# Optimization experiments

Hardware: AMD Instinct MI355X
Metric: run time of the kernel (lower is better)

## Reference

```python
import jax, jax.numpy as jnp
import numpy as np
from functools import partial

TAU = 2.0       # membrane time constant
V_TH = 1.0      # firing threshold
SLOPE = 10.0    # surrogate sigmoid slope (matches rate_encode's 10*)
T = 10          # time_window
H = 12          # num_heads


def lif_step(v, I):
    """One LIF update: leaky integrate, surrogate spike, multiplicative reset."""
    v = v + (I - v) / TAU
    spk = jax.nn.sigmoid(SLOPE * (v - V_TH))
    v = v * (1.0 - spk)
    return spk, v


def setup_inputs() -> dict:
    key = jax.random.key(0)
    ks = jax.random.split(key, 5)
    B, S, E = 8, 1024, 768
    scale = 1.0 / np.sqrt(E)
    x = jax.random.uniform(ks[0], (B, S, E), dtype=jnp.float32)
    Wq = jax.random.normal(ks[1], (E, E), dtype=jnp.float32) * scale
    Wk = jax.random.normal(ks[2], (E, E), dtype=jnp.float32) * scale
    Wv = jax.random.normal(ks[3], (E, E), dtype=jnp.float32) * scale
    Wo = jax.random.normal(ks[4], (E, E), dtype=jnp.float32) * scale
    zb = jnp.zeros((E,), dtype=jnp.float32)
    return {"x": x, "Wq": Wq, "bq": zb, "Wk": Wk, "bk": zb,
            "Wv": Wv, "bv": zb, "Wo": Wo, "bo": zb}


def reference(x, Wq, bq, Wk, bk, Wv, bv, Wo, bo):
    B, S, E = x.shape
    D = E // H
    # rate encoding probability (x assumed in [0,1] range, clipped)
    p = jnp.clip(x, 0.0, 1.0)  # [B,S,E]

    def step(carry, t):
        vq, vk, vv, Qa, Ka, Va = carry
        inp = jax.nn.sigmoid(SLOPE * (p * T - t))  # [B,S,E] spikes at step t
        qs, vq = lif_step(vq, inp @ Wq.T + bq)
        ks, vk = lif_step(vk, inp @ Wk.T + bk)
        vs, vv = lif_step(vv, inp @ Wv.T + bv)
        return (vq, vk, vv, Qa + qs, Ka + ks, Va + vs), None

    z = jnp.zeros((B, S, E), dtype=x.dtype)
    t_idx = jnp.arange(T, dtype=x.dtype)
    (vq, vk, vv, Q, K, V), _ = jax.lax.scan(step, (z, z, z, z, z, z), t_idx)

    # split heads: [B,S,E] -> [B,H,S,D]
    Qh = Q.reshape(B, S, H, D)
    Kh = K.reshape(B, S, H, D)
    Vh = V.reshape(B, S, H, D)
    scores = jnp.einsum('bqhd,bkhd->bhqk', Qh, Kh) / np.sqrt(D)
    attn = jax.nn.softmax(scores, axis=-1)
    out_h = jnp.einsum('bhqk,bkhd->bqhd', attn, Vh)  # [B,S,H,D]
    out = out_h.reshape(B, S, E)
    # output LIF projection with fresh (zero) state
    out_spk, _ = lif_step(jnp.zeros_like(out), out @ Wo.T + bo)
    return out_spk
```

## Files before the change

### kernel.cpp

```cpp
#include <hip/hip_runtime.h>
#include <math.h>

constexpr int B_ = 8, S_ = 1024, E_ = 768, H_ = 12, D_ = 64, T_ = 10;
constexpr int N_ = B_ * S_;
constexpr int NE_ = N_ * E_;
constexpr int WE_ = E_ * E_;

typedef __attribute__((ext_vector_type(8))) short bf16x8;
typedef __attribute__((ext_vector_type(4))) float f32x4;

#define MFMA16(a,b,c) __builtin_amdgcn_mfma_f32_16x16x32_bf16(a,b,c,0,0,0)

__device__ __forceinline__ float sigm(float z){ return 1.f/(1.f+__expf(-z)); }
__device__ __forceinline__ unsigned short f2bf(float f){
    unsigned int u = __float_as_uint(f);
    u += 0x7FFFu + ((u>>16)&1u);
    return (unsigned short)(u>>16);
}
__device__ __forceinline__ float bf2f(unsigned short h){
    return __uint_as_float(((unsigned int)h)<<16);
}
__device__ __forceinline__ void gl16(const void* g, void* l){
    __builtin_amdgcn_global_load_lds((const __attribute__((address_space(1))) unsigned int*)g,
                                     (__attribute__((address_space(3))) unsigned int*)l, 16, 0, 0);
}

__global__ __launch_bounds__(256) void encode_k(const float* __restrict__ x,
                                                unsigned short* __restrict__ enc){
    const int i = blockIdx.x*256 + threadIdx.x;
    const float4 a = ((const float4*)x)[2*i];
    const float4 b = ((const float4*)x)[2*i+1];
    float p[8] = {a.x,a.y,a.z,a.w,b.x,b.y,b.z,b.w};
#pragma unroll
    for (int e=0;e<8;++e) p[e] = 100.f*fminf(fmaxf(p[e],0.f),1.f);
#pragma unroll
    for (int t=0;t<T_;++t){
        unsigned int w[4];
#pragma unroll
        for (int e=0;e<4;++e){
            unsigned short u0 = f2bf(sigm(p[2*e]   - 10.f*(float)t));
            unsigned short u1 = f2bf(sigm(p[2*e+1] - 10.f*(float)t));
            w[e] = (unsigned int)u0 | ((unsigned int)u1<<16);
        }
        ((uint4*)(enc + (long)t*NE_))[i] = make_uint4(w[0],w[1],w[2],w[3]);
    }
}

__global__ __launch_bounds__(256) void wsplit_k(const float* __restrict__ Wq, const float* __restrict__ Wk,
        const float* __restrict__ Wv, const float* __restrict__ Wo,
        unsigned short* __restrict__ whi, unsigned short* __restrict__ wlo){
    int gi = blockIdx.x*256 + threadIdx.x;
    int z = gi / (WE_/8);
    int r = gi % (WE_/8);
    const float* W = z==0?Wq : z==1?Wk : z==2?Wv : Wo;
    const float4 a = ((const float4*)W)[2*r];
    const float4 b = ((const float4*)W)[2*r+1];
    float f[8]={a.x,a.y,a.z,a.w,b.x,b.y,b.z,b.w};
    unsigned int h[4], l[4];
#pragma unroll
    for (int e=0;e<4;++e){
        unsigned short h0=f2bf(f[2*e]),   l0=f2bf(f[2*e]  -bf2f(h0));
        unsigned short h1=f2bf(f[2*e+1]), l1=f2bf(f[2*e+1]-bf2f(h1));
        h[e] = (unsigned)h0 | ((unsigned)h1<<16);
        l[e] = (unsigned)l0 | ((unsigned)l1<<16);
    }
    ((uint4*)(whi + (long)z*WE_))[r] = make_uint4(h[0],h[1],h[2],h[3]);
    ((uint4*)(wlo + (long)z*WE_))[r] = make_uint4(l[0],l[1],l[2],l[3]);
}

__global__ __launch_bounds__(256,2) void qkv_k(const unsigned short* __restrict__ enc,
        const unsigned short* __restrict__ whi,
        const float* __restrict__ bq, const float* __restrict__ bk, const float* __restrict__ bv,
        float* __restrict__ Qf, float* __restrict__ Kf, float* __restrict__ Vf){
    const int z = blockIdx.z;
    const unsigned short* Wh = whi + (long)z*WE_;
    const float* bias = z==0?bq : z==1?bk : bv;
    float* Out = z==0?Qf : z==1?Kf : Vf;
    const int row0 = blockIdx.x*128, col0 = blockIdx.y*64;

    __shared__ unsigned short Ab[128*64];
    __shared__ unsigned short Bh[64*64];

    const int tid = threadIdx.x, lane = tid&63, wid = tid>>6;
    const int l15 = lane&15, l4 = lane>>4, l7 = lane&7;
    const int wr = wid>>1, wc = wid&1;

    int aSrc[4], bSrc[2];
#pragma unroll
    for (int s=0;s<4;++s){
        int idx = (wid + s*4)*64 + lane;
        int row = idx>>3, ch = idx&7;
        aSrc[s] = (row0+row)*E_ + ((ch ^ (row&7))<<3);
    }
#pragma unroll
    for (int s=0;s<2;++s){
        int idx = (wid + s*4)*64 + lane;
        int row = idx>>3, ch = idx&7;
        bSrc[s] = (col0+row)*E_ + ((ch ^ (row&7))<<3);
    }

    const int aBase = (wr*64 + l15)*128;
    const int bBase = (wc*32 + l15)*128;
    const int sw[2] = { ((l4^l7)<<4), ((((4+l4))^l7)<<4) };

    f32x4 acc[4][2];
    float vm[4][2][4] = {};
    float qa[4][2][4] = {};
    float bn[2];
#pragma unroll
    for (int n=0;n<2;++n) bn[n] = bias[col0 + wc*32 + n*16 + l15];
    const f32x4 zero4 = {0.f,0.f,0.f,0.f};

    for (int t=0;t<T_;++t){
        const long tb = (long)t*NE_;
#pragma unroll
        for (int m=0;m<4;++m)
#pragma unroll
            for (int n=0;n<2;++n) acc[m][n] = zero4;
        for (int kt=0;kt<12;++kt){
            const int k0 = kt*64;
            __syncthreads();
#pragma unroll
            for (int s=0;s<4;++s)
                gl16(enc + tb + aSrc[s] + k0, &Ab[(wid+s*4)*512]);
#pragma unroll
            for (int s=0;s<2;++s)
                gl16(Wh + bSrc[s] + k0, &Bh[(wid+s*4)*512]);
            __syncthreads();
#pragma unroll
            for (int kk=0;kk<2;++kk){
                bf16x8 af[4], fbh[2];
#pragma unroll
                for (int m=0;m<4;++m)
                    af[m] = *(const bf16x8*)((const char*)Ab + aBase + m*2048 + sw[kk]);
#pragma unroll
                for (int n=0;n<2;++n)
                    fbh[n] = *(const bf16x8*)((const char*)Bh + bBase + n*2048 + sw[kk]);
#pragma unroll
                for (int m=0;m<4;++m)
#pragma unroll
                    for (int n=0;n<2;++n)
                        acc[m][n] = MFMA16(af[m], fbh[n], acc[m][n]);
            }
        }
#pragma unroll
        for (int m=0;m<4;++m)
#pragma unroll
            for (int n=0;n<2;++n)
#pragma unroll
                for (int j=0;j<4;++j){
                    float I = acc[m][n][j] + bn[n];
                    float v = (vm[m][n][j] + I)*0.5f;
                    float s = sigm(10.f*v - 10.f);
                    vm[m][n][j] = v*(1.f - s);
                    qa[m][n][j] += s;
                }
    }
#pragma unroll
    for (int m=0;m<4;++m)
#pragma unroll
        for (int n=0;n<2;++n)
#pragma unroll
            for (int j=0;j<4;++j){
                int row = row0 + wr*64 + m*16 + l4*4 + j;
                int col = col0 + wc*32 + n*16 + l15;
                Out[(long)row*E_ + col] = qa[m][n][j];
            }
}

__global__ __launch_bounds__(256) void splitqk_k(const float* __restrict__ Qf, const float* __restrict__ Kf,
        unsigned short* __restrict__ Qh, unsigned short* __restrict__ Ql,
        unsigned short* __restrict__ Kh, unsigned short* __restrict__ Kl){
    const long gi = (long)blockIdx.x*256 + threadIdx.x;
    const float* src = blockIdx.y==0 ? Qf : Kf;
    unsigned short* oh = blockIdx.y==0 ? Qh : Kh;
    unsigned short* ol = blockIdx.y==0 ? Ql : Kl;
    const float4 a = ((const float4*)src)[2*gi];
    const float4 b = ((const float4*)src)[2*gi+1];
    float f[8]={a.x,a.y,a.z,a.w,b.x,b.y,b.z,b.w};
    unsigned int hw[4], lw[4];
#pragma unroll
    for (int e=0;e<4;++e){
        unsigned short h0=f2bf(f[2*e]),   l0=f2bf(f[2*e]  -bf2f(h0));
        unsigned short h1=f2bf(f[2*e+1]), l1=f2bf(f[2*e+1]-bf2f(h1));
        hw[e] = (unsigned)h0 | ((unsigned)h1<<16);
        lw[e] = (unsigned)l0 | ((unsigned)l1<<16);
    }
    ((uint4*)oh)[gi] = make_uint4(hw[0],hw[1],hw[2],hw[3]);
    ((uint4*)ol)[gi] = make_uint4(lw[0],lw[1],lw[2],lw[3]);
}

__global__ __launch_bounds__(256) void vtrans_k(const float* __restrict__ Vf,
        unsigned short* __restrict__ Vth, unsigned short* __restrict__ Vtl){
    __shared__ unsigned short lh[64][68], ll[64][68];
    const int tid = threadIdx.x;
    const long base = ((long)blockIdx.z*S_ + blockIdx.x*64)*E_ + blockIdx.y*64;

    {
        const int key = tid>>2, dq = tid&3;
        const float* p = Vf + base + (long)key*E_ + dq*16;
        float4 v0=((const float4*)p)[0], v1=((const float4*)p)[1];
        float4 v2=((const float4*)p)[2], v3=((const float4*)p)[3];
        float f[16]={v0.x,v0.y,v0.z,v0.w,v1.x,v1.y,v1.z,v1.w,
                     v2.x,v2.y,v2.z,v2.w,v3.x,v3.y,v3.z,v3.w};
#pragma unroll
        for (int i=0;i<8;++i){
            unsigned short h0=f2bf(f[2*i]),   l0=f2bf(f[2*i]  -bf2f(h0));
            unsigned short h1=f2bf(f[2*i+1]), l1=f2bf(f[2*i+1]-bf2f(h1));
            *(unsigned int*)&lh[key][dq*16+2*i] = (unsigned)h0 | ((unsigned)h1<<16);
            *(unsigned int*)&ll[key][dq*16+2*i] = (unsigned)l0 | ((unsigned)l1<<16);
        }
    }
    __syncthreads();
    {
        const int d = tid>>2, kq = tid&3;
        unsigned int hw[8], lw[8];
#pragma unroll
        for (int i=0;i<8;++i){
            unsigned short h0 = lh[kq*16+2*i][d],   h1 = lh[kq*16+2*i+1][d];
            unsigned short l0 = ll[kq*16+2*i][d],   l1 = ll[kq*16+2*i+1][d];
            hw[i] = (unsigned)h0 | ((unsigned)h1<<16);
            lw[i] = (unsigned)l0 | ((unsigned)l1<<16);
        }
        long o = ((long)(blockIdx.z*12 + blockIdx.y))*65536 + (long)d*1024
               + blockIdx.x*64 + kq*16;
        ((uint4*)&Vth[o])[0] = make_uint4(hw[0],hw[1],hw[2],hw[3]);
        ((uint4*)&Vth[o])[1] = make_uint4(hw[4],hw[5],hw[6],hw[7]);
        ((uint4*)&Vtl[o])[0] = make_uint4(lw[0],lw[1],lw[2],lw[3]);
        ((uint4*)&Vtl[o])[1] = make_uint4(lw[4],lw[5],lw[6],lw[7]);
    }
}

__global__ __launch_bounds__(256,2) void attn_k2(
        const unsigned short* __restrict__ Qh_g, const unsigned short* __restrict__ Ql_g,
        const unsigned short* __restrict__ Kh_g, const unsigned short* __restrict__ Kl_g,
        const unsigned short* __restrict__ Vth_g, const unsigned short* __restrict__ Vtl_g,
        unsigned short* __restrict__ atth, unsigned short* __restrict__ attl){
    const int q0 = blockIdx.x*64;
    const int h  = blockIdx.y;
    const int b  = blockIdx.z;
    const long base = ((long)b*S_)*E_ + h*64;
    const long vtb  = (long)(b*12 + h) * 65536;

    __shared__ char smem[65536];
    unsigned short* QhL = (unsigned short*)(smem);
    unsigned short* QlL = (unsigned short*)(smem + 8192);
    unsigned short* KhL = (unsigned short*)(smem + 16384);
    unsigned short* KlL = (unsigned short*)(smem + 24576);
    unsigned short* VhL = (unsigned short*)(smem + 32768);
    unsigned short* VlL = (unsigned short*)(smem + 40960);
    unsigned short* Ph = (unsigned short*)(smem + 49152);
    unsigned short* Pl = (unsigned short*)(smem + 57344);
    float* OT = (float*)(smem + 16384);

    const int tid = threadIdx.x, lane = tid&63, wid = tid>>6;
    const int l15 = lane&15, l4 = lane>>4, l7 = lane&7;
    const int qrow = wid*16 + l15;

    int sOff[2], vOff[2];
#pragma unroll
    for (int s=0;s<2;++s){
        int idx = (wid + s*4)*64 + lane;
        int r = idx>>3, c = idx&7;
        sOff[s] = r*E_ + ((c ^ (r&7))<<3);
        vOff[s] = (r<<10) + ((c ^ (r&7))<<3);
    }

#pragma unroll
    for (int s=0;s<2;++s){
        gl16(Qh_g + base + (long)q0*E_ + sOff[s], &QhL[(wid+s*4)*512]);
        gl16(Ql_g + base + (long)q0*E_ + sOff[s], &QlL[(wid+s*4)*512]);
    }
    __syncthreads();
    bf16x8 qfh[2], qfl[2];
#pragma unroll
    for (int kk=0;kk<2;++kk){
        int off = qrow*128 + ((((kk<<2)+l4) ^ l7)<<4);
        qfh[kk] = *(const bf16x8*)((const char*)QhL + off);
        qfl[kk] = *(const bf16x8*)((const char*)QlL + off);
    }

    float mrun = -1e30f, lrun = 0.f;
    f32x4 ot[4];
    const f32x4 zero4 = {0.f,0.f,0.f,0.f};
#pragma unroll
    for (int m=0;m<4;++m) ot[m] = zero4;

    for (int kt=0;kt<16;++kt){
        const int k0 = kt*64;
        __syncthreads();
#pragma unroll
        for (int s=0;s<2;++s){
            gl16(Kh_g + base + (long)k0*E_ + sOff[s], &KhL[(wid+s*4)*512]);
            gl16(Kl_g + base + (long)k0*E_ + sOff[s], &KlL[(wid+s*4)*512]);
            gl16(Vth_g + vtb + k0 + vOff[s], &VhL[(wid+s*4)*512]);
            gl16(Vtl_g + vtb + k0 + vOff[s], &VlL[(wid+s*4)*512]);
        }
        __syncthreads();
        f32x4 st[4];
#pragma unroll
        for (int m=0;m<4;++m) st[m] = zero4;
#pragma unroll
        for (int kk=0;kk<2;++kk){
            int swo = ((((kk<<2)+l4) ^ l7)<<4);
            bf16x8 kh[4], kl2[4];
#pragma unroll
            for (int m=0;m<4;++m){
                int off = (m*16+l15)*128 + swo;
                kh[m]  = *(const bf16x8*)((const char*)KhL + off);
                kl2[m] = *(const bf16x8*)((const char*)KlL + off);
            }
#pragma unroll
            for (int m=0;m<4;++m){
                st[m] = MFMA16(kh[m],  qfh[kk], st[m]);
                st[m] = MFMA16(kh[m],  qfl[kk], st[m]);
                st[m] = MFMA16(kl2[m], qfh[kk], st[m]);
            }
        }
        float pmax = -1e30f;
#pragma unroll
        for (int m=0;m<4;++m)
#pragma unroll
            for (int j=0;j<4;++j){ st[m][j] *= 0.125f; pmax = fmaxf(pmax, st[m][j]); }
        pmax = fmaxf(pmax, __shfl_xor(pmax,16));
        pmax = fmaxf(pmax, __shfl_xor(pmax,32));
        float mnew = fmaxf(mrun, pmax);
        float alpha = __expf(mrun - mnew);
        float p[16]; float psum = 0.f;
#pragma unroll
        for (int m=0;m<4;++m)
#pragma unroll
            for (int j=0;j<4;++j){ float e = __expf(st[m][j]-mnew); p[m*4+j]=e; psum+=e; }
        psum += __shfl_xor(psum,16);
        psum += __shfl_xor(psum,32);
        lrun = lrun*alpha + psum;
        mrun = mnew;
#pragma unroll
        for (int m=0;m<4;++m)
#pragma unroll
            for (int j=0;j<4;++j) ot[m][j] *= alpha;
#pragma unroll
        for (int m=0;m<4;++m)
#pragma unroll
            for (int jp=0;jp<2;++jp){
                float fx = p[m*4+jp*2], fy = p[m*4+jp*2+1];
                unsigned short hx=f2bf(fx), hy=f2bf(fy);
                unsigned short lx=f2bf(fx-bf2f(hx)), ly=f2bf(fy-bf2f(hy));
                int key = m*16 + l4*4 + jp*2;
                int byte = qrow*128 + ((key<<1) ^ (l7<<4));
                *(unsigned int*)((char*)Ph + byte) = (unsigned)hx | ((unsigned)hy<<16);
                *(unsigned int*)((char*)Pl + byte) = (unsigned)lx | ((unsigned)ly<<16);
            }
#pragma unroll
        for (int kk=0;kk<2;++kk){
            int swo = ((((kk<<2)+l4) ^ l7)<<4);
            bf16x8 pfh = *(const bf16x8*)((const char*)Ph + qrow*128 + swo);
            bf16x8 pfl = *(const bf16x8*)((const char*)Pl + qrow*128 + swo);
#pragma unroll
            for (int m=0;m<4;++m){
                int off = (m*16+l15)*128 + swo;
                bf16x8 vvh = *(const bf16x8*)((const char*)VhL + off);
                bf16x8 vvl = *(const bf16x8*)((const char*)VlL + off);
                ot[m] = MFMA16(vvh, pfh, ot[m]);
                ot[m] = MFMA16(vvh, pfl, ot[m]);
                ot[m] = MFMA16(vvl, pfh, ot[m]);
            }
        }
    }
    __syncthreads();
    float inv = 1.f/lrun;
#pragma unroll
    for (int m=0;m<4;++m)
#pragma unroll
        for (int j=0;j<4;++j){
            int d = m*16 + l4*4 + j;
            OT[qrow*68 + d] = ot[m][j]*inv;
        }
    __syncthreads();
    {
        int q = tid>>2, d0 = (tid&3)*16;
        const float* rp = OT + q*68 + d0;
        float4 f0=((const float4*)rp)[0], f1=((const float4*)rp)[1];
        float4 f2=((const float4*)rp)[2], f3=((const float4*)rp)[3];
        float f[16]={f0.x,f0.y,f0.z,f0.w,f1.x,f1.y,f1.z,f1.w,f2.x,f2.y,f2.z,f2.w,f3.x,f3.y,f3.z,f3.w};
        bf16x8 vh[2], vl[2];
#pragma unroll
        for (int g=0;g<2;++g)
#pragma unroll
            for (int e=0;e<8;++e){
                unsigned short hh = f2bf(f[g*8+e]);
                vh[g][e] = (short)hh;
                vl[g][e] = (short)f2bf(f[g*8+e]-bf2f(hh));
            }
        long o = base + (long)(q0+q)*E_ + d0;
        *(bf16x8*)(atth + o)     = vh[0];
        *(bf16x8*)(atth + o + 8) = vh[1];
        *(bf16x8*)(attl + o)     = vl[0];
        *(bf16x8*)(attl + o + 8) = vl[1];
    }
}

__global__ __launch_bounds__(256,2) void out_k(const unsigned short* __restrict__ Ah_g,
        const unsigned short* __restrict__ Al_g,
        const unsigned short* __restrict__ Wh,
        const float* __restrict__ bias, float* __restrict__ out){
    const int row0 = blockIdx.x*128, col0 = blockIdx.y*64;
    __shared__ unsigned short Ah[128*64], Al[128*64];
    __shared__ unsigned short Bh2[64*64];

    const int tid = threadIdx.x, lane = tid&63, wid = tid>>6;
    const int l15 = lane&15, l4 = lane>>4, l7 = lane&7;
    const int wr = wid>>1, wc = wid&1;

    int aSrc[4], bSrc[2];
#pragma unroll
    for (int s=0;s<4;++s){
        int idx = (wid + s*4)*64 + lane;
        int row = idx>>3, ch = idx&7;
        aSrc[s] = (row0+row)*E_ + ((ch ^ (row&7))<<3);
    }
#pragma unroll
    for (int s=0;s<2;++s){
        int idx = (wid + s*4)*64 + lane;
        int row = idx>>3, ch = idx&7;
        bSrc[s] = (col0+row)*E_ + ((ch ^ (row&7))<<3);
    }
    const int aBase = (wr*64 + l15)*128;
    const int bBase = (wc*32 + l15)*128;
    const int sw[2] = { ((l4^l7)<<4), ((((4+l4))^l7)<<4) };

    f32x4 acc[4][2];
    const f32x4 zero4 = {0.f,0.f,0.f,0.f};
#pragma unroll
    for (int m=0;m<4;++m)
#pragma unroll
        for (int n=0;n<2;++n) acc[m][n] = zero4;

    for (int kt=0;kt<12;++kt){
        const int k0 = kt*64;
        __syncthreads();
#pragma unroll
        for (int s=0;s<4;++s){
            gl16(Ah_g + aSrc[s] + k0, &Ah[(wid+s*4)*512]);
            gl16(Al_g + aSrc[s] + k0, &Al[(wid+s*4)*512]);
        }
#pragma unroll
        for (int s=0;s<2;++s)
            gl16(Wh + bSrc[s] + k0, &Bh2[(wid+s*4)*512]);
        __syncthreads();
#pragma unroll
        for (int kk=0;kk<2;++kk){
            bf16x8 ah[4], al[4], fbh[2];
#pragma unroll
            for (int m=0;m<4;++m){
                ah[m] = *(const bf16x8*)((const char*)Ah + aBase + m*2048 + sw[kk]);
                al[m] = *(const bf16x8*)((const char*)Al + aBase + m*2048 + sw[kk]);
            }
#pragma unroll
            for (int n=0;n<2;++n)
                fbh[n] = *(const bf16x8*)((const char*)Bh2 + bBase + n*2048 + sw[kk]);
#pragma unroll
            for (int m=0;m<4;++m)
#pragma unroll
                for (int n=0;n<2;++n){
                    acc[m][n] = MFMA16(ah[m], fbh[n], acc[m][n]);
                    acc[m][n] = MFMA16(al[m], fbh[n], acc[m][n]);
                }
        }
    }
#pragma unroll
    for (int m=0;m<4;++m)
#pragma unroll
        for (int n=0;n<2;++n){
            float bn = bias[col0 + wc*32 + n*16 + l15];
#pragma unroll
            for (int j=0;j<4;++j){
                int row = row0 + wr*64 + m*16 + l4*4 + j;
                int col = col0 + wc*32 + n*16 + l15;
                float I = acc[m][n][j] + bn;
                out[(long)row*E_ + col] = sigm(5.f*I - 10.f);
            }
        }
}

extern "C" void kernel_launch(void* const* d_in, const int* in_sizes, int n_in,
                              void* d_out, int out_size, void* d_ws, size_t ws_size,
                              hipStream_t stream){
    const float* x  = (const float*)d_in[0];
    const float* Wq = (const float*)d_in[1];
    const float* bq = (const float*)d_in[2];
    const float* Wk = (const float*)d_in[3];
    const float* bk = (const float*)d_in[4];
    const float* Wv = (const float*)d_in[5];
    const float* bv = (const float*)d_in[6];
    const float* Wo = (const float*)d_in[7];
    const float* bo = (const float*)d_in[8];
    float* out = (float*)d_out;

    char* ws = (char*)d_ws;
    unsigned short* enc  = (unsigned short*)ws;
    unsigned short* atth = (unsigned short*)ws;
    unsigned short* attl = (unsigned short*)(ws + (long)NE_*2);
    unsigned short* Qh_g  = (unsigned short*)(ws + 25165824L);
    unsigned short* Ql_g  = Qh_g + NE_;
    unsigned short* Kh_g  = Ql_g + NE_;
    unsigned short* Kl_g  = Kh_g + NE_;
    unsigned short* Vth_g = Kl_g + NE_;
    unsigned short* Vtl_g = Vth_g + NE_;
    unsigned short* whi  = (unsigned short*)(ws + 125829120L);
    unsigned short* wlo  = whi + 4L*WE_;
    float* Qf = (float*)(ws + 135266304L);
    float* Kf = Qf + NE_;
    float* Vf = Kf + NE_;

    wsplit_k<<<dim3(4*(WE_/8)/256), 256, 0, stream>>>(Wq,Wk,Wv,Wo,whi,wlo);
    encode_k<<<dim3(NE_/8/256), 256, 0, stream>>>(x,enc);
    qkv_k<<<dim3(64,12,3), 256, 0, stream>>>(enc,whi,bq,bk,bv,Qf,Kf,Vf);
    splitqk_k<<<dim3(NE_/8/256, 2), 256, 0, stream>>>(Qf,Kf,Qh_g,Ql_g,Kh_g,Kl_g);
    vtrans_k<<<dim3(16,12,8), 256, 0, stream>>>(Vf,Vth_g,Vtl_g);
    attn_k2<<<dim3(16,12,8), 256, 0, stream>>>(Qh_g,Ql_g,Kh_g,Kl_g,Vth_g,Vtl_g,
                                               atth,attl);
    out_k<<<dim3(64,12), 256, 0, stream>>>(atth,attl,whi+3L*WE_,bo,out);
}
```

Baseline: 585.3 us.

## Double-buffer LDS tiles in QKV GEMM with async prefetch across timesteps

Converts the QKV spiking GEMM kernel to double-buffered LDS. The next K-tile, or the first tile of the next timestep, is issued with global_load_lds before computing on the current tile, and manual vmcnt waits plus raw barriers replace the two __syncthreads per iteration. It also raises the launch-bounds occupancy hint from 2 to 3 and bumps wave priority during the MFMA phase. The goal is to hide global-memory latency behind MFMA work, at the cost of doubled shared memory and possible register pressure under the tighter occupancy bound.

```diff
diff --git a/kernel.cpp b/kernel.cpp
--- a/kernel.cpp
+++ b/kernel.cpp
@@ -68,7 +68,7 @@
     ((uint4*)(wlo + (long)z*WE_))[r] = make_uint4(l[0],l[1],l[2],l[3]);
 }
 
-__global__ __launch_bounds__(256,2) void qkv_k(const unsigned short* __restrict__ enc,
+__global__ __launch_bounds__(256,3) void qkv_k(const unsigned short* __restrict__ enc,
         const unsigned short* __restrict__ whi,
         const float* __restrict__ bq, const float* __restrict__ bk, const float* __restrict__ bv,
         float* __restrict__ Qf, float* __restrict__ Kf, float* __restrict__ Vf){
@@ -78,8 +78,8 @@
     float* Out = z==0?Qf : z==1?Kf : Vf;
     const int row0 = blockIdx.x*128, col0 = blockIdx.y*64;
 
-    __shared__ unsigned short Ab[128*64];
-    __shared__ unsigned short Bh[64*64];
+    __shared__ unsigned short Ab[2][128*64];
+    __shared__ unsigned short Bh[2][64*64];
 
     const int tid = threadIdx.x, lane = tid&63, wid = tid>>6;
     const int l15 = lane&15, l4 = lane>>4, l7 = lane&7;
@@ -109,39 +109,59 @@
     float bn[2];
 #pragma unroll
     for (int n=0;n<2;++n) bn[n] = bias[col0 + wc*32 + n*16 + l15];
+    asm volatile("" :: "v"(bn[0]), "v"(bn[1]));
     const f32x4 zero4 = {0.f,0.f,0.f,0.f};
 
+#define STAGE(tt, kk2, slot)                                               \
+    do {                                                                   \
+        const unsigned short* eb_ = enc + (long)(tt)*NE_ + (kk2)*64;       \
+        _Pragma("unroll")                                                  \
+        for (int s_=0;s_<4;++s_)                                           \
+            gl16(eb_ + aSrc[s_], &Ab[slot][(wid+s_*4)*512]);               \
+        _Pragma("unroll")                                                  \
+        for (int s_=0;s_<2;++s_)                                           \
+            gl16(Wh + bSrc[s_] + (kk2)*64, &Bh[slot][(wid+s_*4)*512]);     \
+    } while(0)
+
+    STAGE(0, 0, 0);
+
     for (int t=0;t<T_;++t){
-        const long tb = (long)t*NE_;
 #pragma unroll
         for (int m=0;m<4;++m)
 #pragma unroll
             for (int n=0;n<2;++n) acc[m][n] = zero4;
+#pragma unroll
         for (int kt=0;kt<12;++kt){
-            const int k0 = kt*64;
-            __syncthreads();
-#pragma unroll
-            for (int s=0;s<4;++s)
-                gl16(enc + tb + aSrc[s] + k0, &Ab[(wid+s*4)*512]);
-#pragma unroll
-            for (int s=0;s<2;++s)
-                gl16(Wh + bSrc[s] + k0, &Bh[(wid+s*4)*512]);
-            __syncthreads();
+            const int slotC = kt&1;
+            const int slotS = slotC^1;
+            if (kt < 11){
+                STAGE(t, kt+1, slotS);
+                asm volatile("s_waitcnt vmcnt(6)" ::: "memory");
+            } else if (t < 9){
+                STAGE(t+1, 0, slotS);
+                asm volatile("s_waitcnt vmcnt(6)" ::: "memory");
+            } else {
+                asm volatile("s_waitcnt vmcnt(0)" ::: "memory");
+            }
+            __builtin_amdgcn_s_barrier();
+            __builtin_amdgcn_s_setprio(1);
 #pragma unroll
             for (int kk=0;kk<2;++kk){
                 bf16x8 af[4], fbh[2];
 #pragma unroll
                 for (int m=0;m<4;++m)
-                    af[m] = *(const bf16x8*)((const char*)Ab + aBase + m*2048 + sw[kk]);
+                    af[m] = *(const bf16x8*)((const char*)&Ab[slotC][0] + aBase + m*2048 + sw[kk]);
 #pragma unroll
                 for (int n=0;n<2;++n)
-                    fbh[n] = *(const bf16x8*)((const char*)Bh + bBase + n*2048 + sw[kk]);
+                    fbh[n] = *(const bf16x8*)((const char*)&Bh[slotC][0] + bBase + n*2048 + sw[kk]);
 #pragma unroll
                 for (int m=0;m<4;++m)
 #pragma unroll
                     for (int n=0;n<2;++n)
                         acc[m][n] = MFMA16(af[m], fbh[n], acc[m][n]);
             }
+            __builtin_amdgcn_s_setprio(0);
+            __builtin_amdgcn_s_barrier();
         }
 #pragma unroll
         for (int m=0;m<4;++m)
@@ -156,6 +176,7 @@
                     qa[m][n][j] += s;
                 }
     }
+#undef STAGE
 #pragma unroll
     for (int m=0;m<4;++m)
 #pragma unroll
```

New measurement: 700.2 us. 19.6% more time.
